# Performance work log

Measured on AMD Instinct MI355X. Metric: run time of the kernel, lower is better.

Reference implementation:

```python
import jax, jax.numpy as jnp
import numpy as np

N = 100000      # nodes
E = 1600000     # edges
G = 128         # graphs in batch
D_IN = 20       # node_feat_dim
D_EMB = 300     # emb_dim
D_OUT = 64      # output_feats
L_REST = 4      # layers 1..4 (num_layers=5 total)
BN_EPS = 1e-5


def setup_inputs() -> dict:
    key = jax.random.key(0)
    ks = jax.random.split(key, 24)
    s = 0.05
    node_feats = jax.random.normal(ks[0], (N, D_IN), jnp.float32)
    edge_feats = jax.random.normal(ks[1], (E, 1), jnp.float32)
    src = jax.random.randint(ks[2], (E,), 0, N, dtype=jnp.int32)
    dst = jax.random.randint(ks[3], (E,), 0, N, dtype=jnp.int32)
    graph_ids = jnp.sort(jax.random.randint(ks[4], (N,), 0, G, dtype=jnp.int32))
    # layer 0: D_IN -> 2*D_EMB -> D_EMB, BN(D_EMB)
    w1_0 = jax.random.normal(ks[5], (D_IN, 2 * D_EMB), jnp.float32) * s
    b1_0 = jnp.zeros((2 * D_EMB,), jnp.float32)
    w2_0 = jax.random.normal(ks[6], (2 * D_EMB, D_EMB), jnp.float32) * s
    b2_0 = jnp.zeros((D_EMB,), jnp.float32)
    gamma_0 = jnp.ones((D_EMB,), jnp.float32)
    beta_0 = jnp.zeros((D_EMB,), jnp.float32)
    # layers 1..4: D_EMB -> 2*D_EMB -> D_EMB, BN(D_EMB), stacked
    w1 = jax.random.normal(ks[7], (L_REST, D_EMB, 2 * D_EMB), jnp.float32) * s
    b1 = jnp.zeros((L_REST, 2 * D_EMB), jnp.float32)
    w2 = jax.random.normal(ks[8], (L_REST, 2 * D_EMB, D_EMB), jnp.float32) * s
    b2 = jnp.zeros((L_REST, D_EMB), jnp.float32)
    gamma = jnp.ones((L_REST, D_EMB), jnp.float32)
    beta = jnp.zeros((L_REST, D_EMB), jnp.float32)
    # final transform Linear(300, 64)
    wt = jax.random.normal(ks[9], (D_EMB, D_OUT), jnp.float32) * s
    bt = jnp.zeros((D_OUT,), jnp.float32)
    return {"node_feats": node_feats, "edge_feats": edge_feats, "src": src,
            "dst": dst, "graph_ids": graph_ids,
            "w1_0": w1_0, "b1_0": b1_0, "w2_0": w2_0, "b2_0": b2_0,
            "gamma_0": gamma_0, "beta_0": beta_0,
            "w1": w1, "b1": b1, "w2": w2, "b2": b2,
            "gamma": gamma, "beta": beta, "wt": wt, "bt": bt}


def _gin_layer(x, e, src, dst, w1, b1, w2, b2, g, b):
    # u_add_e: gather source node feats, add (broadcast) edge feats -> [E, d]
    m = x[src] + e
    # sum aggregation to destination nodes -> [N, d]
    agg = jax.ops.segment_sum(m, dst, num_segments=N)
    # MLP: Linear -> ReLU -> Linear
    h = jnp.maximum(agg @ w1 + b1, 0.0) @ w2 + b2
    # BatchNorm1d with batch statistics (biased var), affine
    mu = h.mean(axis=0)
    var = h.var(axis=0)
    h = (h - mu) * jax.lax.rsqrt(var + BN_EPS) * g + b
    return h  # no activation (GINLayer activation=None); dropout is eval-mode identity


def reference(node_feats, edge_feats, src, dst, graph_ids,
              w1_0, b1_0, w2_0, b2_0, gamma_0, beta_0,
              w1, b1, w2, b2, gamma, beta, wt, bt):
    h = _gin_layer(node_feats, edge_feats, src, dst,
                   w1_0, b1_0, w2_0, b2_0, gamma_0, beta_0)
    for l in range(L_REST):
        h = _gin_layer(h, edge_feats, src, dst,
                       w1[l], b1[l], w2[l], b2[l], gamma[l], beta[l])
    # AvgPooling readout per graph
    sums = jax.ops.segment_sum(h, graph_ids, num_segments=G)          # [G, D_EMB]
    counts = jax.ops.segment_sum(jnp.ones((N,), h.dtype), graph_ids, num_segments=G)
    graph_feats = sums / jnp.maximum(counts, 1.0)[:, None]
    return graph_feats @ wt + bt  # [G, D_OUT]
```

## Files before the change

### kernel.cpp

```cpp
#include <hip/hip_runtime.h>

#define NN 100000
#define NE 1600000
#define NG 128
#define DIN 20
#define DEMB 300
#define DHID 600
#define DOUT 64
#define DIN_P 32
#define EMB_P 320
#define HID_P 640
#define EMB_G 384
#define SCAN_BLK 392

static const float BN_EPS_F = 1e-5f;

typedef _Float16 f16x8 __attribute__((ext_vector_type(8)));
typedef float f32x4 __attribute__((ext_vector_type(4)));

__device__ __forceinline__ void gload_lds16(const void* g, const void* l) {
  __builtin_amdgcn_global_load_lds(
      (const __attribute__((address_space(1))) unsigned int*)(unsigned long long)g,
      (__attribute__((address_space(3))) unsigned int*)(unsigned long long)(unsigned int)(unsigned long long)l,
      16, 0, 0);
}


__global__ void count_edges_kernel(const int* __restrict__ dst, const float* __restrict__ ef,
                                   int* __restrict__ counts, float* __restrict__ esum) {
  int e = blockIdx.x * blockDim.x + threadIdx.x;
  if (e >= NE) return;
  int v = dst[e];
  atomicAdd(&counts[v], 1);
  atomicAdd(&esum[v], ef[e]);
}

__global__ __launch_bounds__(256) void scan_part1(const int* __restrict__ counts,
                                                  int* __restrict__ bsums) {
  __shared__ int red[256];
  int t = threadIdx.x;
  int i = blockIdx.x * 256 + t;
  red[t] = (i < NN) ? counts[i] : 0;
  __syncthreads();
  for (int s = 128; s > 0; s >>= 1) {
    if (t < s) red[t] += red[t + s];
    __syncthreads();
  }
  if (t == 0) bsums[blockIdx.x] = red[0];
}

__global__ __launch_bounds__(512) void scan_part2(const int* __restrict__ bsums,
                                                  int* __restrict__ boffs) {
  __shared__ int sc[512];
  int t = threadIdx.x;
  int v = (t < SCAN_BLK) ? bsums[t] : 0;
  sc[t] = v;
  __syncthreads();
  for (int off = 1; off < 512; off <<= 1) {
    int u = (t >= off) ? sc[t - off] : 0;
    __syncthreads();
    sc[t] += u;
    __syncthreads();
  }
  if (t < SCAN_BLK) boffs[t] = sc[t] - v;
}

__global__ __launch_bounds__(256) void scan_part3(const int* __restrict__ counts,
                                                  const int* __restrict__ boffs,
                                                  int* __restrict__ row_ptr,
                                                  int* __restrict__ cursor) {
  __shared__ int sc[256];
  int t = threadIdx.x;
  int i = blockIdx.x * 256 + t;
  int v = (i < NN) ? counts[i] : 0;
  sc[t] = v;
  __syncthreads();
  for (int off = 1; off < 256; off <<= 1) {
    int u = (t >= off) ? sc[t - off] : 0;
    __syncthreads();
    sc[t] += u;
    __syncthreads();
  }
  if (i < NN) {
    int excl = sc[t] - v + boffs[blockIdx.x];
    row_ptr[i] = excl;
    cursor[i] = excl;
  }
  if (i == NN - 1) row_ptr[NN] = NE;
}

__global__ void scatter_kernel(const int* __restrict__ src, const int* __restrict__ dst,
                               int* __restrict__ cursor, int* __restrict__ csr_src) {
  int e = blockIdx.x * blockDim.x + threadIdx.x;
  if (e >= NE) return;
  int pos = atomicAdd(&cursor[dst[e]], 1);
  csr_src[pos] = src[e];
}


__global__ void repack_wt_kernel(const float* __restrict__ w, _Float16* __restrict__ out,
                                 int K, int Nsrc, int Np, int Kp) {
  int idx = blockIdx.x * blockDim.x + threadIdx.x;
  if (idx >= Np * Kp) return;
  int n = idx / Kp, k = idx - n * Kp;
  float v = (n < Nsrc && k < K) ? w[(size_t)k * Nsrc + n] : 0.f;
  out[idx] = (_Float16)v;
}

__global__ void pad_bias_kernel(const float* __restrict__ b, float* __restrict__ out, int n, int np) {
  int i = blockIdx.x * blockDim.x + threadIdx.x;
  if (i >= np) return;
  out[i] = (i < n) ? b[i] : 0.f;
}


__global__ __launch_bounds__(256) void spmm0_kernel(const float* __restrict__ x,
                                                    const int* __restrict__ row_ptr,
                                                    const int* __restrict__ csr_src,
                                                    const float* __restrict__ esum,
                                                    _Float16* __restrict__ out) {
  int wid = (blockIdx.x * blockDim.x + threadIdx.x) >> 6;
  int lane = threadIdx.x & 63;
  if (wid >= NN) return;
  int beg = row_ptr[wid], end = row_ptr[wid + 1];
  float acc = 0.f;
  int j = beg;
  for (; j + 1 < end; j += 2) {
    int s0 = csr_src[j], s1 = csr_src[j + 1];
    if (lane < DIN) {
      acc += x[(size_t)s0 * DIN + lane];
      acc += x[(size_t)s1 * DIN + lane];
    }
  }
  if (j < end) {
    int s0 = csr_src[j];
    if (lane < DIN) acc += x[(size_t)s0 * DIN + lane];
  }
  if (lane < DIN_P) {
    float v = (lane < DIN) ? acc + esum[wid] : 0.f;
    out[(size_t)wid * DIN_P + lane] = (_Float16)v;
  }
}


__global__ __launch_bounds__(256) void spmm_f16_kernel(const _Float16* __restrict__ x,
                                                       const float* __restrict__ scale,
                                                       const float* __restrict__ shift,
                                                       const int* __restrict__ row_ptr,
                                                       const int* __restrict__ csr_src,
                                                       const float* __restrict__ esum,
                                                       _Float16* __restrict__ out) {
  int wid = (blockIdx.x * blockDim.x + threadIdx.x) >> 6;
  int lane = threadIdx.x & 63;
  if (wid >= NN) return;
  int beg = row_ptr[wid], end = row_ptr[wid + 1];
  float deg = (float)(end - beg);
  float es = esum[wid];
  if (lane >= 40) return;
  const f16x8* xb = (const f16x8*)x;
  float acc[8] = {};
  int j = beg;
  for (; j + 7 < end; j += 8) {
    int s0 = csr_src[j + 0], s1 = csr_src[j + 1], s2 = csr_src[j + 2], s3 = csr_src[j + 3];
    int s4 = csr_src[j + 4], s5 = csr_src[j + 5], s6 = csr_src[j + 6], s7 = csr_src[j + 7];
    f16x8 v0 = xb[(size_t)s0 * 40 + lane];
    f16x8 v1 = xb[(size_t)s1 * 40 + lane];
    f16x8 v2 = xb[(size_t)s2 * 40 + lane];
    f16x8 v3 = xb[(size_t)s3 * 40 + lane];
    f16x8 v4 = xb[(size_t)s4 * 40 + lane];
    f16x8 v5 = xb[(size_t)s5 * 40 + lane];
    f16x8 v6 = xb[(size_t)s6 * 40 + lane];
    f16x8 v7 = xb[(size_t)s7 * 40 + lane];
#pragma unroll
    for (int i = 0; i < 8; ++i) {
      acc[i] += ((float)v0[i] + (float)v1[i]) + ((float)v2[i] + (float)v3[i]) +
                ((float)v4[i] + (float)v5[i]) + ((float)v6[i] + (float)v7[i]);
    }
  }
  for (; j < end; ++j) {
    f16x8 v0 = xb[(size_t)csr_src[j] * 40 + lane];
#pragma unroll
    for (int i = 0; i < 8; ++i) acc[i] += (float)v0[i];
  }
  int c = lane * 8;
  f16x8 o;
#pragma unroll
  for (int i = 0; i < 8; ++i)
    o[i] = (_Float16)(acc[i] * scale[c + i] + deg * shift[c + i] + es);
  ((f16x8*)(out))[(size_t)wid * 40 + lane] = o;
}


template <bool RELU, bool STATS>
__global__ __launch_bounds__(256) void gemm_lds_kernel(const _Float16* __restrict__ A,
                                                       const _Float16* __restrict__ Bt,
                                                       const float* __restrict__ bias,
                                                       _Float16* __restrict__ C,
                                                       int M, int K, int ldC, int NREAL,
                                                       float* __restrict__ stats) {
  __shared__ _Float16 lds[16 * 512];
  const int t = threadIdx.x;
  const int wv = t >> 6;
  const int lane = t & 63;
  const int fm = lane & 15;
  const int k8 = (lane >> 4) * 8;
  const int m0 = blockIdx.y * 128;
  const int n0 = blockIdx.x * 128;
  const int wmq = (wv >> 1) * 4;
  const int wnq = (wv & 1) * 4;

  const _Float16* ApS[2];
  const _Float16* BpS[2];
#pragma unroll
  for (int i = 0; i < 2; ++i) {
    int mi = 2 * wv + i;
    int r = min(m0 + mi * 16 + fm, M - 1);
    ApS[i] = A + (size_t)r * K + k8;
    BpS[i] = Bt + (size_t)(n0 + mi * 16 + fm) * K + k8;
  }

  f32x4 acc[4][4] = {};

  for (int k0 = 0; k0 < K; k0 += 32) {
#pragma unroll
    for (int i = 0; i < 2; ++i) {
      int mi = 2 * wv + i;
      gload_lds16(ApS[i] + k0, &lds[mi * 512 + lane * 8]);
      gload_lds16(BpS[i] + k0, &lds[(8 + mi) * 512 + lane * 8]);
    }
    __syncthreads();
    f16x8 a[4], b[4];
#pragma unroll
    for (int i = 0; i < 4; ++i) a[i] = *(const f16x8*)&lds[(wmq + i) * 512 + lane * 8];
#pragma unroll
    for (int i = 0; i < 4; ++i) b[i] = *(const f16x8*)&lds[(8 + wnq + i) * 512 + lane * 8];
#pragma unroll
    for (int mi = 0; mi < 4; ++mi)
#pragma unroll
      for (int ni = 0; ni < 4; ++ni)
        acc[mi][ni] = __builtin_amdgcn_mfma_f32_16x16x32_f16(a[mi], b[ni], acc[mi][ni], 0, 0, 0);
    __syncthreads();
  }

  float bi[4];
#pragma unroll
  for (int ni = 0; ni < 4; ++ni) bi[ni] = bias[n0 + (wnq + ni) * 16 + fm];
  const int rq = (lane >> 4) * 4;
  float ssum[4] = {}, ssq[4] = {};
#pragma unroll
  for (int mi = 0; mi < 4; ++mi) {
#pragma unroll
    for (int ni = 0; ni < 4; ++ni) {
      int col = n0 + (wnq + ni) * 16 + fm;
#pragma unroll
      for (int r = 0; r < 4; ++r) {
        int row = m0 + (wmq + mi) * 16 + rq + r;
        float v = acc[mi][ni][r] + bi[ni];
        if (RELU) v = fmaxf(v, 0.f);
        if (row < M && col < NREAL) C[(size_t)row * ldC + col] = (_Float16)v;
        if (STATS && row < M) { ssum[ni] += v; ssq[ni] += v * v; }
      }
    }
  }
  if (STATS) {
    float* sred = (float*)lds;
    if (t < 128) { sred[t] = 0.f; sred[128 + t] = 0.f; }
    __syncthreads();
    const int wn = (wv & 1) * 64;
#pragma unroll
    for (int ni = 0; ni < 4; ++ni) {
      atomicAdd(&sred[wn + ni * 16 + fm], ssum[ni]);
      atomicAdd(&sred[128 + wn + ni * 16 + fm], ssq[ni]);
    }
    __syncthreads();
    if (t < 128) {
      int gc = blockIdx.x * 128 + t;
      atomicAdd(&stats[gc], sred[t]);
      atomicAdd(&stats[EMB_G + gc], sred[128 + t]);
    }
  }
}


__global__ void bn_finalize_kernel(const float* __restrict__ stats, const float* __restrict__ gamma,
                                   const float* __restrict__ beta, float* __restrict__ scale,
                                   float* __restrict__ shift) {
  int c = threadIdx.x;
  if (c >= EMB_G) return;
  if (c < DEMB) {
    float mu = stats[c] / (float)NN;
    float var = fmaxf(stats[EMB_G + c] / (float)NN - mu * mu, 0.f);
    float sc = gamma[c] * rsqrtf(var + BN_EPS_F);
    scale[c] = sc;
    shift[c] = beta[c] - mu * sc;
  } else {
    scale[c] = 0.f;
    shift[c] = 0.f;
  }
}


#define POOL_BLOCKS 784

__global__ __launch_bounds__(256) void pool2_kernel(const _Float16* __restrict__ h,
                                                    const int* __restrict__ gid,
                                                    float* __restrict__ graw) {
  const int w = (blockIdx.x * 256 + threadIdx.x) >> 6;
  const int lane = threadIdx.x & 63;
  const int NW = POOL_BLOCKS * 4;
  const int rpw = (NN + NW - 1) / NW;
  int r0 = w * rpw, r1 = min(r0 + rpw, NN);
  if (r0 >= r1 || lane >= 40) return;
  const f16x8* hb = (const f16x8*)h;
  float acc[8] = {};
  int curg = gid[r0];
  for (int r = r0; r < r1; ++r) {
    int g = gid[r];
    if (g != curg) {
#pragma unroll
      for (int i = 0; i < 8; ++i) {
        atomicAdd(&graw[curg * EMB_P + lane * 8 + i], acc[i]);
        acc[i] = 0.f;
      }
      curg = g;
    }
    f16x8 v = hb[(size_t)r * 40 + lane];
#pragma unroll
    for (int i = 0; i < 8; ++i) acc[i] += (float)v[i];
  }
#pragma unroll
  for (int i = 0; i < 8; ++i) atomicAdd(&graw[curg * EMB_P + lane * 8 + i], acc[i]);
}

__global__ void final_kernel(const float* __restrict__ graw, const int* __restrict__ gid,
                             const float* __restrict__ scale, const float* __restrict__ shift,
                             const float* __restrict__ wt, const float* __restrict__ bt,
                             float* __restrict__ out) {
  int g = blockIdx.x, t = threadIdx.x;
  __shared__ int sb[2];
  if (t < 2) {
    int target = g + t;
    int lo = 0, hi = NN;
    while (lo < hi) {
      int m = (lo + hi) >> 1;
      if (gid[m] < target) lo = m + 1; else hi = m;
    }
    sb[t] = lo;
  }
  __syncthreads();
  int cnt = sb[1] - sb[0];
  float inv = cnt > 0 ? 1.0f / (float)cnt : 0.f;
  float sh_on = cnt > 0 ? 1.0f : 0.f;
  float acc = bt[t];
  const float* row = graw + g * EMB_P;
  for (int k = 0; k < DEMB; ++k) {
    float gf = row[k] * inv * scale[k] + sh_on * shift[k];
    acc = fmaf(gf, wt[k * DOUT + t], acc);
  }
  out[g * DOUT + t] = acc;
}


extern "C" void kernel_launch(void* const* d_in, const int* in_sizes, int n_in,
                              void* d_out, int out_size, void* d_ws, size_t ws_size,
                              hipStream_t stream) {
  const float* node_feats = (const float*)d_in[0];
  const float* edge_feats = (const float*)d_in[1];
  const int* src = (const int*)d_in[2];
  const int* dst = (const int*)d_in[3];
  const int* gid = (const int*)d_in[4];
  const float* w1_0 = (const float*)d_in[5];
  const float* b1_0 = (const float*)d_in[6];
  const float* w2_0 = (const float*)d_in[7];
  const float* b2_0 = (const float*)d_in[8];
  const float* gamma_0 = (const float*)d_in[9];
  const float* beta_0 = (const float*)d_in[10];
  const float* w1s = (const float*)d_in[11];
  const float* b1s = (const float*)d_in[12];
  const float* w2s = (const float*)d_in[13];
  const float* b2s = (const float*)d_in[14];
  const float* gammas = (const float*)d_in[15];
  const float* betas = (const float*)d_in[16];
  const float* wt = (const float*)d_in[17];
  const float* bt = (const float*)d_in[18];
  float* out = (float*)d_out;
  (void)in_sizes; (void)n_in; (void)out_size; (void)ws_size;

  char* ws = (char*)d_ws;
  size_t off = 0;
  auto carve = [&](size_t bytes) -> void* {
    void* p = ws + off;
    off += (bytes + 255) & ~(size_t)255;
    return p;
  };
  _Float16* P0 = (_Float16*)carve((size_t)NN * EMB_P * 2);
  _Float16* P1 = (_Float16*)carve((size_t)NN * EMB_P * 2);
  _Float16* Q  = (_Float16*)carve((size_t)NN * HID_P * 2);
  float* esum   = (float*)carve((size_t)NN * 4);
  int* counts   = (int*)carve((size_t)NN * 4);
  int* row_ptr  = (int*)carve((size_t)(NN + 1) * 4);
  int* cursor   = (int*)carve((size_t)NN * 4);
  int* csr_src  = (int*)carve((size_t)NE * 4);
  int* bsums    = (int*)carve((size_t)SCAN_BLK * 4);
  int* boffs    = (int*)carve((size_t)SCAN_BLK * 4);
  _Float16* w1t0 = (_Float16*)carve((size_t)HID_P * DIN_P * 2);
  _Float16* w1t  = (_Float16*)carve((size_t)4 * HID_P * EMB_P * 2);
  _Float16* w2t  = (_Float16*)carve((size_t)5 * EMB_G * HID_P * 2);
  float* b1p   = (float*)carve((size_t)5 * HID_P * 4);
  float* b2p   = (float*)carve((size_t)5 * EMB_G * 4);
  float* stats = (float*)carve(2 * EMB_G * 4);
  float* scale = (float*)carve(EMB_G * 4);
  float* shift = (float*)carve(EMB_G * 4);
  float* graw  = (float*)carve((size_t)NG * EMB_P * 4);

  hipMemsetAsync(esum, 0, (size_t)NN * 4, stream);
  hipMemsetAsync(counts, 0, (size_t)NN * 4, stream);
  hipMemsetAsync(graw, 0, (size_t)NG * EMB_P * 4, stream);

  count_edges_kernel<<<(NE + 255) / 256, 256, 0, stream>>>(dst, edge_feats, counts, esum);
  scan_part1<<<SCAN_BLK, 256, 0, stream>>>(counts, bsums);
  scan_part2<<<1, 512, 0, stream>>>(bsums, boffs);
  scan_part3<<<SCAN_BLK, 256, 0, stream>>>(counts, boffs, row_ptr, cursor);
  scatter_kernel<<<(NE + 255) / 256, 256, 0, stream>>>(src, dst, cursor, csr_src);

  repack_wt_kernel<<<(HID_P * DIN_P + 255) / 256, 256, 0, stream>>>(w1_0, w1t0, DIN, DHID, HID_P, DIN_P);
  for (int l = 0; l < 4; ++l) {
    repack_wt_kernel<<<(HID_P * EMB_P + 255) / 256, 256, 0, stream>>>(
        w1s + (size_t)l * DEMB * DHID, w1t + (size_t)l * HID_P * EMB_P, DEMB, DHID, HID_P, EMB_P);
  }
  repack_wt_kernel<<<(EMB_G * HID_P + 255) / 256, 256, 0, stream>>>(w2_0, w2t, DHID, DEMB, EMB_G, HID_P);
  for (int l = 0; l < 4; ++l) {
    repack_wt_kernel<<<(EMB_G * HID_P + 255) / 256, 256, 0, stream>>>(
        w2s + (size_t)l * DHID * DEMB, w2t + (size_t)(l + 1) * EMB_G * HID_P, DHID, DEMB, EMB_G, HID_P);
  }
  pad_bias_kernel<<<(HID_P + 255) / 256, 256, 0, stream>>>(b1_0, b1p, DHID, HID_P);
  pad_bias_kernel<<<(EMB_G + 255) / 256, 256, 0, stream>>>(b2_0, b2p, DEMB, EMB_G);
  for (int l = 0; l < 4; ++l) {
    pad_bias_kernel<<<(HID_P + 255) / 256, 256, 0, stream>>>(b1s + (size_t)l * DHID, b1p + (size_t)(l + 1) * HID_P, DHID, HID_P);
    pad_bias_kernel<<<(EMB_G + 255) / 256, 256, 0, stream>>>(b2s + (size_t)l * DEMB, b2p + (size_t)(l + 1) * EMB_G, DEMB, EMB_G);
  }

  const int MT = (NN + 127) / 128;
  const int spmm_blocks = (NN * 64 + 255) / 256;

  for (int l = 0; l < 5; ++l) {
    const _Float16* w1t_l = (l == 0) ? w1t0 : w1t + (size_t)(l - 1) * HID_P * EMB_P;
    const _Float16* w2t_l = w2t + (size_t)l * EMB_G * HID_P;
    const float* b1p_l = b1p + (size_t)l * HID_P;
    const float* b2p_l = b2p + (size_t)l * EMB_G;
    const float* ga = (l == 0) ? gamma_0 : gammas + (size_t)(l - 1) * DEMB;
    const float* be = (l == 0) ? beta_0 : betas + (size_t)(l - 1) * DEMB;
    int K1 = (l == 0) ? DIN_P : EMB_P;

    if (l == 0) {
      spmm0_kernel<<<spmm_blocks, 256, 0, stream>>>(node_feats, row_ptr, csr_src, esum, P0);
    } else {
      spmm_f16_kernel<<<spmm_blocks, 256, 0, stream>>>(P1, scale, shift, row_ptr, csr_src, esum, P0);
    }

    gemm_lds_kernel<true, false><<<dim3(HID_P / 128, MT), 256, 0, stream>>>(
        P0, w1t_l, b1p_l, Q, NN, K1, HID_P, HID_P, nullptr);

    hipMemsetAsync(stats, 0, 2 * EMB_G * 4, stream);
    gemm_lds_kernel<false, true><<<dim3(EMB_G / 128, MT), 256, 0, stream>>>(
        Q, w2t_l, b2p_l, P1, NN, HID_P, EMB_P, EMB_P, stats);

    bn_finalize_kernel<<<1, EMB_G, 0, stream>>>(stats, ga, be, scale, shift);
  }

  pool2_kernel<<<POOL_BLOCKS, 256, 0, stream>>>(P1, gid, graw);
  final_kernel<<<NG, 64, 0, stream>>>(graw, gid, scale, shift, wt, bt, out);
}
```

Measured before the change: 2.414 ms.

## Restructure GEMM to stage B panel in LDS and stream A from registers

Replaces the 128x128 LDS-tiled GEMM with a 128x64 tile. A K-stage of up to 320 of the weight panel is loaded into LDS once per stage, and each wave streams its own A rows straight from global memory into registers with a one-step prefetch. Output padding shrinks from 384 to 320 columns, which removes the wasted MFMA work on padded columns in the second GEMM. This cuts LDS traffic for A and the per-k barriers, at the cost of re-reading A rows across more column blocks, uncoalesced direct A loads, and a large LDS footprint that limits occupancy.

```diff
diff --git a/kernel.cpp b/kernel.cpp
--- a/kernel.cpp
+++ b/kernel.cpp
@@ -10,8 +10,8 @@
 #define DIN_P 32
 #define EMB_P 320
 #define HID_P 640
-#define EMB_G 384
 #define SCAN_BLK 392
+#define KSTG 320
 
 static const float BN_EPS_F = 1e-5f;
 
@@ -192,91 +192,102 @@
 
 
 template <bool RELU, bool STATS>
-__global__ __launch_bounds__(256) void gemm_lds_kernel(const _Float16* __restrict__ A,
-                                                       const _Float16* __restrict__ Bt,
-                                                       const float* __restrict__ bias,
-                                                       _Float16* __restrict__ C,
-                                                       int M, int K, int ldC, int NREAL,
-                                                       float* __restrict__ stats) {
-  __shared__ _Float16 lds[16 * 512];
+__global__ __launch_bounds__(256, 4) void gemm_blds_kernel(const _Float16* __restrict__ A,
+                                                           const _Float16* __restrict__ Bt,
+                                                           const float* __restrict__ bias,
+                                                           _Float16* __restrict__ C,
+                                                           int M, int K, int ldC,
+                                                           float* __restrict__ stats) {
+  __shared__ __align__(16) _Float16 lds[64 * KSTG];
   const int t = threadIdx.x;
   const int wv = t >> 6;
   const int lane = t & 63;
   const int fm = lane & 15;
   const int k8 = (lane >> 4) * 8;
   const int m0 = blockIdx.y * 128;
-  const int n0 = blockIdx.x * 128;
-  const int wmq = (wv >> 1) * 4;
-  const int wnq = (wv & 1) * 4;
-
-  const _Float16* ApS[2];
-  const _Float16* BpS[2];
-#pragma unroll
-  for (int i = 0; i < 2; ++i) {
-    int mi = 2 * wv + i;
-    int r = min(m0 + mi * 16 + fm, M - 1);
-    ApS[i] = A + (size_t)r * K + k8;
-    BpS[i] = Bt + (size_t)(n0 + mi * 16 + fm) * K + k8;
-  }
-
-  f32x4 acc[4][4] = {};
-
-  for (int k0 = 0; k0 < K; k0 += 32) {
-#pragma unroll
-    for (int i = 0; i < 2; ++i) {
-      int mi = 2 * wv + i;
-      gload_lds16(ApS[i] + k0, &lds[mi * 512 + lane * 8]);
-      gload_lds16(BpS[i] + k0, &lds[(8 + mi) * 512 + lane * 8]);
-    }
-    __syncthreads();
-    f16x8 a[4], b[4];
-#pragma unroll
-    for (int i = 0; i < 4; ++i) a[i] = *(const f16x8*)&lds[(wmq + i) * 512 + lane * 8];
-#pragma unroll
-    for (int i = 0; i < 4; ++i) b[i] = *(const f16x8*)&lds[(8 + wnq + i) * 512 + lane * 8];
-#pragma unroll
-    for (int mi = 0; mi < 4; ++mi)
-#pragma unroll
-      for (int ni = 0; ni < 4; ++ni)
-        acc[mi][ni] = __builtin_amdgcn_mfma_f32_16x16x32_f16(a[mi], b[ni], acc[mi][ni], 0, 0, 0);
-    __syncthreads();
-  }
+  const int n0 = blockIdx.x * 64;
+
+  const _Float16* Ap[2];
+#pragma unroll
+  for (int rg = 0; rg < 2; ++rg) {
+    int r = min(m0 + wv * 32 + rg * 16 + fm, M - 1);
+    Ap[rg] = A + (size_t)r * K + k8;
+  }
+
+  f32x4 acc[2][4] = {};
+  const int nkc_tot = K >> 5;
+
+  for (int ks0 = 0; ks0 < K; ks0 += KSTG) {
+    const int klen = min(KSTG, K - ks0);
+    const int nkc = klen >> 5;
+    const int NCH = nkc << 2;
+    for (int c = wv; c < NCH; c += 4) {
+      int kc = c >> 2, ni = c & 3;
+      gload_lds16(Bt + (size_t)(n0 + ni * 16 + fm) * K + ks0 + kc * 32 + k8,
+                  &lds[c * 512 + lane * 8]);
+    }
+    __syncthreads();
+
+    f16x8 a[2];
+    a[0] = *(const f16x8*)(Ap[0] + ks0);
+    a[1] = *(const f16x8*)(Ap[1] + ks0);
+    for (int kc = 0; kc < nkc; ++kc) {
+      f16x8 an[2];
+      int knext = ks0 + (kc + 1) * 32;
+      if (knext < K) {
+        an[0] = *(const f16x8*)(Ap[0] + knext);
+        an[1] = *(const f16x8*)(Ap[1] + knext);
+      }
+      f16x8 b[4];
+#pragma unroll
+      for (int ni = 0; ni < 4; ++ni) b[ni] = *(const f16x8*)&lds[(kc * 4 + ni) * 512 + lane * 8];
+#pragma unroll
+      for (int rg = 0; rg < 2; ++rg)
+#pragma unroll
+        for (int ni = 0; ni < 4; ++ni)
+          acc[rg][ni] = __builtin_amdgcn_mfma_f32_16x16x32_f16(a[rg], b[ni], acc[rg][ni], 0, 0, 0);
+      if (knext < K) { a[0] = an[0]; a[1] = an[1]; }
+    }
+    if (ks0 + KSTG < K) __syncthreads();
+  }
+  (void)nkc_tot;
 
   float bi[4];
 #pragma unroll
-  for (int ni = 0; ni < 4; ++ni) bi[ni] = bias[n0 + (wnq + ni) * 16 + fm];
+  for (int ni = 0; ni < 4; ++ni) bi[ni] = bias[n0 + ni * 16 + fm];
   const int rq = (lane >> 4) * 4;
   float ssum[4] = {}, ssq[4] = {};
 #pragma unroll
-  for (int mi = 0; mi < 4; ++mi) {
+  for (int rg = 0; rg < 2; ++rg) {
 #pragma unroll
     for (int ni = 0; ni < 4; ++ni) {
-      int col = n0 + (wnq + ni) * 16 + fm;
+      int col = n0 + ni * 16 + fm;
 #pragma unroll
       for (int r = 0; r < 4; ++r) {
-        int row = m0 + (wmq + mi) * 16 + rq + r;
-        float v = acc[mi][ni][r] + bi[ni];
+        int row = m0 + wv * 32 + rg * 16 + rq + r;
+        float v = acc[rg][ni][r] + bi[ni];
         if (RELU) v = fmaxf(v, 0.f);
-        if (row < M && col < NREAL) C[(size_t)row * ldC + col] = (_Float16)v;
-        if (STATS && row < M) { ssum[ni] += v; ssq[ni] += v * v; }
+        if (row < M) {
+          C[(size_t)row * ldC + col] = (_Float16)v;
+          if (STATS) { ssum[ni] += v; ssq[ni] += v * v; }
+        }
       }
     }
   }
   if (STATS) {
+    __syncthreads();
     float* sred = (float*)lds;
-    if (t < 128) { sred[t] = 0.f; sred[128 + t] = 0.f; }
-    __syncthreads();
-    const int wn = (wv & 1) * 64;
+    if (t < 128) sred[t] = 0.f;
+    __syncthreads();
 #pragma unroll
     for (int ni = 0; ni < 4; ++ni) {
-      atomicAdd(&sred[wn + ni * 16 + fm], ssum[ni]);
-      atomicAdd(&sred[128 + wn + ni * 16 + fm], ssq[ni]);
-    }
-    __syncthreads();
-    if (t < 128) {
-      int gc = blockIdx.x * 128 + t;
-      atomicAdd(&stats[gc], sred[t]);
-      atomicAdd(&stats[EMB_G + gc], sred[128 + t]);
+      atomicAdd(&sred[ni * 16 + fm], ssum[ni]);
+      atomicAdd(&sred[64 + ni * 16 + fm], ssq[ni]);
+    }
+    __syncthreads();
+    if (t < 64) {
+      atomicAdd(&stats[n0 + t], sred[t]);
+      atomicAdd(&stats[EMB_P + n0 + t], sred[64 + t]);
     }
   }
 }
@@ -286,10 +297,10 @@
                                    const float* __restrict__ beta, float* __restrict__ scale,
                                    float* __restrict__ shift) {
   int c = threadIdx.x;
-  if (c >= EMB_G) return;
+  if (c >= EMB_P) return;
   if (c < DEMB) {
     float mu = stats[c] / (float)NN;
-    float var = fmaxf(stats[EMB_G + c] / (float)NN - mu * mu, 0.f);
+    float var = fmaxf(stats[EMB_P + c] / (float)NN - mu * mu, 0.f);
     float sc = gamma[c] * rsqrtf(var + BN_EPS_F);
     scale[c] = sc;
     shift[c] = beta[c] - mu * sc;
@@ -405,12 +416,12 @@
   int* boffs    = (int*)carve((size_t)SCAN_BLK * 4);
   _Float16* w1t0 = (_Float16*)carve((size_t)HID_P * DIN_P * 2);
   _Float16* w1t  = (_Float16*)carve((size_t)4 * HID_P * EMB_P * 2);
-  _Float16* w2t  = (_Float16*)carve((size_t)5 * EMB_G * HID_P * 2);
+  _Float16* w2t  = (_Float16*)carve((size_t)5 * EMB_P * HID_P * 2);
   float* b1p   = (float*)carve((size_t)5 * HID_P * 4);
-  float* b2p   = (float*)carve((size_t)5 * EMB_G * 4);
-  float* stats = (float*)carve(2 * EMB_G * 4);
-  float* scale = (float*)carve(EMB_G * 4);
-  float* shift = (float*)carve(EMB_G * 4);
+  float* b2p   = (float*)carve((size_t)5 * EMB_P * 4);
+  float* stats = (float*)carve(2 * EMB_P * 4);
+  float* scale = (float*)carve(EMB_P * 4);
+  float* shift = (float*)carve(EMB_P * 4);
   float* graw  = (float*)carve((size_t)NG * EMB_P * 4);
 
   hipMemsetAsync(esum, 0, (size_t)NN * 4, stream);
@@ -428,16 +439,16 @@
     repack_wt_kernel<<<(HID_P * EMB_P + 255) / 256, 256, 0, stream>>>(
         w1s + (size_t)l * DEMB * DHID, w1t + (size_t)l * HID_P * EMB_P, DEMB, DHID, HID_P, EMB_P);
   }
-  repack_wt_kernel<<<(EMB_G * HID_P + 255) / 256, 256, 0, stream>>>(w2_0, w2t, DHID, DEMB, EMB_G, HID_P);
+  repack_wt_kernel<<<(EMB_P * HID_P + 255) / 256, 256, 0, stream>>>(w2_0, w2t, DHID, DEMB, EMB_P, HID_P);
   for (int l = 0; l < 4; ++l) {
-    repack_wt_kernel<<<(EMB_G * HID_P + 255) / 256, 256, 0, stream>>>(
-        w2s + (size_t)l * DHID * DEMB, w2t + (size_t)(l + 1) * EMB_G * HID_P, DHID, DEMB, EMB_G, HID_P);
+    repack_wt_kernel<<<(EMB_P * HID_P + 255) / 256, 256, 0, stream>>>(
+        w2s + (size_t)l * DHID * DEMB, w2t + (size_t)(l + 1) * EMB_P * HID_P, DHID, DEMB, EMB_P, HID_P);
   }
   pad_bias_kernel<<<(HID_P + 255) / 256, 256, 0, stream>>>(b1_0, b1p, DHID, HID_P);
-  pad_bias_kernel<<<(EMB_G + 255) / 256, 256, 0, stream>>>(b2_0, b2p, DEMB, EMB_G);
+  pad_bias_kernel<<<(EMB_P + 255) / 256, 256, 0, stream>>>(b2_0, b2p, DEMB, EMB_P);
   for (int l = 0; l < 4; ++l) {
     pad_bias_kernel<<<(HID_P + 255) / 256, 256, 0, stream>>>(b1s + (size_t)l * DHID, b1p + (size_t)(l + 1) * HID_P, DHID, HID_P);
-    pad_bias_kernel<<<(EMB_G + 255) / 256, 256, 0, stream>>>(b2s + (size_t)l * DEMB, b2p + (size_t)(l + 1) * EMB_G, DEMB, EMB_G);
+    pad_bias_kernel<<<(EMB_P + 255) / 256, 256, 0, stream>>>(b2s + (size_t)l * DEMB, b2p + (size_t)(l + 1) * EMB_P, DEMB, EMB_P);
   }
 
   const int MT = (NN + 127) / 128;
@@ -445,9 +456,9 @@
 
   for (int l = 0; l < 5; ++l) {
     const _Float16* w1t_l = (l == 0) ? w1t0 : w1t + (size_t)(l - 1) * HID_P * EMB_P;
-    const _Float16* w2t_l = w2t + (size_t)l * EMB_G * HID_P;
+    const _Float16* w2t_l = w2t + (size_t)l * EMB_P * HID_P;
     const float* b1p_l = b1p + (size_t)l * HID_P;
-    const float* b2p_l = b2p + (size_t)l * EMB_G;
+    const float* b2p_l = b2p + (size_t)l * EMB_P;
     const float* ga = (l == 0) ? gamma_0 : gammas + (size_t)(l - 1) * DEMB;
     const float* be = (l == 0) ? beta_0 : betas + (size_t)(l - 1) * DEMB;
     int K1 = (l == 0) ? DIN_P : EMB_P;
@@ -458,14 +469,14 @@
       spmm_f16_kernel<<<spmm_blocks, 256, 0, stream>>>(P1, scale, shift, row_ptr, csr_src, esum, P0);
     }
 
-    gemm_lds_kernel<true, false><<<dim3(HID_P / 128, MT), 256, 0, stream>>>(
-        P0, w1t_l, b1p_l, Q, NN, K1, HID_P, HID_P, nullptr);
-
-    hipMemsetAsync(stats, 0, 2 * EMB_G * 4, stream);
-    gemm_lds_kernel<false, true><<<dim3(EMB_G / 128, MT), 256, 0, stream>>>(
-        Q, w2t_l, b2p_l, P1, NN, HID_P, EMB_P, EMB_P, stats);
-
-    bn_finalize_kernel<<<1, EMB_G, 0, stream>>>(stats, ga, be, scale, shift);
+    gemm_blds_kernel<true, false><<<dim3(HID_P / 64, MT), 256, 0, stream>>>(
+        P0, w1t_l, b1p_l, Q, NN, K1, HID_P, nullptr);
+
+    hipMemsetAsync(stats, 0, 2 * EMB_P * 4, stream);
+    gemm_blds_kernel<false, true><<<dim3(EMB_P / 64, MT), 256, 0, stream>>>(
+        Q, w2t_l, b2p_l, P1, NN, HID_P, EMB_P, stats);
+
+    bn_finalize_kernel<<<1, EMB_P, 0, stream>>>(stats, ga, be, scale, shift);
   }
 
   pool2_kernel<<<POOL_BLOCKS, 256, 0, stream>>>(P1, gid, graw);
```

Result: slower. 2.577 ms (+6.7%).
